# Kernel tuning notes

Hardware: AMD Instinct MI355X
Metric: run time of the kernel (lower is better)

The kernel has to match this reference:

```python
import jax, jax.numpy as jnp
import numpy as np

B, P, S = 32, 4096, 128
D_INT, D_VC, D_PATCH, H = 512, 512, 768, 4
D_CONCAT = D_INT + D_VC
D_HEAD = D_CONCAT // H  # 256
TEMPERATURE = 1.0


def setup_inputs() -> dict:
    key = jax.random.key(0)
    ks = jax.random.split(key, 9)
    h_int = jax.random.normal(ks[0], (B, D_INT), dtype=jnp.float32)
    h_vc = jax.random.normal(ks[1], (B, D_VC), dtype=jnp.float32)
    patch_tokens = jax.random.normal(ks[2], (B, P, D_PATCH), dtype=jnp.float32)
    boundaries = jnp.sort(jax.random.randint(ks[3], (S + 1,), 0, P, dtype=jnp.int32))
    # Per-head projection weights (nn.Linear: y = x @ W.T + b)
    qW = jax.random.normal(ks[4], (H, D_HEAD, D_CONCAT), dtype=jnp.float32) / np.sqrt(D_CONCAT)
    qb = jax.random.normal(ks[5], (H, D_HEAD), dtype=jnp.float32) * 0.01
    kW = jax.random.normal(ks[6], (H, D_HEAD, D_PATCH), dtype=jnp.float32) / np.sqrt(D_PATCH)
    kb = jax.random.normal(ks[7], (H, D_HEAD), dtype=jnp.float32) * 0.01
    return {"h_int": h_int, "h_vc": h_vc, "patch_tokens": patch_tokens,
            "boundaries": boundaries, "qW": qW, "qb": qb, "kW": kW, "kb": kb}


def reference(h_int, h_vc, patch_tokens, boundaries, qW, qb, kW, kb):
    b, p, _ = patch_tokens.shape
    s = boundaries.shape[0] - 1
    h_concat = jnp.concatenate([h_int, h_vc], axis=-1)            # [B, d_concat]
    # All heads at once (equivalent to the per-head Python loop)
    q = jnp.einsum('bc,hdc->bhd', h_concat, qW) + qb              # [B, H, d_head]
    k = jnp.einsum('bpc,hdc->bphd', patch_tokens, kW) + kb        # [B, P, H, d_head]
    patch_scores = jnp.einsum('bhd,bphd->bph', q, k)              # [B, P, H]
    # Map each patch to its stroke segment; out-of-range -> dump bucket s
    pos = jnp.arange(p)
    seg = jnp.searchsorted(boundaries, pos, side='right') - 1     # [P]
    seg = jnp.where((seg < 0) | (seg >= s), s, seg)
    st = patch_scores.transpose(1, 0, 2)                          # [P, B, H]
    ssum = jax.ops.segment_sum(st, seg, num_segments=s + 1)[:s]   # [S, B, H]
    cnt = jax.ops.segment_sum(jnp.ones((p,), st.dtype), seg, num_segments=s + 1)[:s]  # [S]
    stroke_scores = ssum / jnp.maximum(cnt, 1.0)[:, None, None]   # mean over patches; 0 if empty
    avg_scores = stroke_scores.mean(axis=-1).transpose(1, 0)      # [B, S] (mean over heads)
    return jax.nn.sigmoid(avg_scores / TEMPERATURE)
```

## Files before the change

### kernel.cpp

```cpp
#include <hip/hip_runtime.h>
#include <math.h>

#define NB 32
#define NP 4096
#define NS 128
#define DI 512
#define DV 512
#define DP 768
#define NH 4
#define DC 1024
#define DH 256

typedef float f4 __attribute__((ext_vector_type(4)));

__global__ __launch_bounds__(256) void k_q2(const float* __restrict__ h_int,
                                            const float* __restrict__ h_vc,
                                            const float* __restrict__ qW,
                                            const float* __restrict__ qb,
                                            const float* __restrict__ kb,
                                            float* __restrict__ q,
                                            float* __restrict__ bavg_part,
                                            float* __restrict__ acc) {
    int b = blockIdx.x >> 4, g = blockIdx.x & 15;
    int tid = threadIdx.x;

    int zi = blockIdx.x * 256 + tid;
    if (zi < NB * (NS + 1)) acc[zi] = 0.f;

    __shared__ float hc[DC];
    for (int i = tid; i < DI; i += 256) hc[i] = h_int[b * DI + i];
    for (int i = tid; i < DV; i += 256) hc[DI + i] = h_vc[b * DV + i];
    __syncthreads();

    int j = tid >> 2, r = tid & 3;
    int o = g * 64 + j;
    const float* w = qW + (size_t)o * DC + r * 256;
    const float* hq = hc + r * 256;
    float s = 0.f;
#pragma unroll 8
    for (int c = 0; c < 256; c += 4) {
        f4 wv = *(const f4*)(w + c);
        s += wv.x * hq[c] + wv.y * hq[c + 1] + wv.z * hq[c + 2] + wv.w * hq[c + 3];
    }
    s += __shfl_xor(s, 1);
    s += __shfl_xor(s, 2);
    float qv = s + qb[o];

    __shared__ float red[64];
    if (r == 0) {
        q[(size_t)b * (NH * DH) + o] = qv;
        red[j] = qv * kb[o];
    }
    __syncthreads();
    if (tid == 0) {
        float t = 0.f;
        for (int i = 0; i < 64; ++i) t += red[i];
        bavg_part[b * 16 + g] = t;
    }
}

__global__ __launch_bounds__(256) void k_w2(const float* __restrict__ q,
                                            const float* __restrict__ kW,
                                            float* __restrict__ w_part) {
    int bid = blockIdx.x;
    int cc = bid % 3, bh = bid / 3;
    int h = bh % NH, b = bh / NH;
    int tid = threadIdx.x;

    __shared__ float qs[DH];
    __shared__ f4 part[4][64];
    if (tid < DH) qs[tid] = q[(size_t)b * (NH * DH) + h * DH + tid];
    __syncthreads();

    int rc = tid >> 6, cg = tid & 63;
    const float* kbase = kW + (size_t)(h * DH + rc * 64) * DP + cc * 256 + cg * 4;
    const float* qr = qs + rc * 64;
    f4 wacc = 0.f;
#pragma unroll 8
    for (int i = 0; i < 64; ++i) {
        f4 kv = *(const f4*)(kbase + (size_t)i * DP);
        wacc += qr[i] * kv;
    }
    part[rc][cg] = wacc;
    __syncthreads();
    if (rc == 0) {
        f4 t = (part[0][cg] + part[1][cg]) + (part[2][cg] + part[3][cg]);
        *(f4*)(w_part + (size_t)(b * NH + h) * DP + cc * 256 + cg * 4) =
            t * (1.0f / NH);
    }
}

__global__ __launch_bounds__(256, 4) void k_score(const float* __restrict__ patch,
                                                  const float* __restrict__ w_part,
                                                  const int* __restrict__ bnd,
                                                  float* __restrict__ acc) {
    constexpr int CHUNKS = 32;
    constexpr int PPB = NP / CHUNKS;
    constexpr int PPW = PPB / 4;
    constexpr int RS = DP / 4;
    int b = blockIdx.x / CHUNKS;
    int chunk = blockIdx.x % CHUNKS;
    __shared__ int bsh[NS + 1];
    int tid = threadIdx.x;
    if (tid <= NS) bsh[tid] = bnd[tid];
    __syncthreads();
    int wave = tid >> 6, lane = tid & 63;

    const f4* wp = (const f4*)(w_part + (size_t)b * NH * DP);
    f4 w0 = 0.f, w1 = 0.f, w2 = 0.f;
#pragma unroll
    for (int h = 0; h < NH; ++h) {
        w0 += wp[h * RS + lane];
        w1 += wp[h * RS + 64 + lane];
        w2 += wp[h * RS + 128 + lane];
    }
    float* accb = acc + (size_t)b * (NS + 1);

    int p0 = chunk * PPB + wave * PPW;

    int cur, nxt;
    if (p0 < bsh[0]) {
        cur = NS; nxt = bsh[0];
    } else {
        int lo = 0, hi = NS;
        while (lo < hi) {
            int mid = (lo + hi + 1) >> 1;
            if (bsh[mid] <= p0) lo = mid; else hi = mid - 1;
        }
        cur = lo;
        nxt = (cur < NS) ? bsh[cur + 1] : NP;
    }

    f4 r0 = 0.f, r1 = 0.f, r2 = 0.f;
    const f4* base = (const f4*)(patch + ((size_t)b * NP + p0) * DP);

#define LOADROW(dst0, dst1, dst2, i)                                          \
    {                                                                         \
        const f4* rp_ = base + (size_t)(i) * RS;                              \
        dst0 = __builtin_nontemporal_load(rp_ + lane);                        \
        dst1 = __builtin_nontemporal_load(rp_ + 64 + lane);                   \
        dst2 = __builtin_nontemporal_load(rp_ + 128 + lane);                  \
    }

#define PROCROW(s0, s1, s2, i)                                                \
    {                                                                         \
        int p_ = p0 + (i);                                                    \
        if (p_ >= nxt) {        \
            f4 sv = r0 * w0 + r1 * w1 + r2 * w2;                              \
            float s = sv.x + sv.y + sv.z + sv.w;                              \
            for (int off_ = 32; off_ > 0; off_ >>= 1) s += __shfl_xor(s, off_); \
            if (lane == 0) atomicAdd(&accb[cur], s);                          \
            r0 = 0.f; r1 = 0.f; r2 = 0.f;                                     \
            cur = (cur == NS) ? 0 : cur + 1;                                  \
            while (cur < NS && bsh[cur + 1] <= p_) cur++;                     \
            nxt = (cur < NS) ? bsh[cur + 1] : NP;                             \
        }                                                                     \
        r0 += s0; r1 += s1; r2 += s2;                                         \
    }

    f4 A0, A1, A2, B0, B1, B2, C0, C1, C2, D0, D1, D2;
    LOADROW(A0, A1, A2, 0)
    LOADROW(B0, B1, B2, 1)
#pragma unroll
    for (int g2 = 0; g2 < PPW - 2; g2 += 2) {
        LOADROW(C0, C1, C2, g2 + 2)
        LOADROW(D0, D1, D2, g2 + 3)
        PROCROW(A0, A1, A2, g2)
        PROCROW(B0, B1, B2, g2 + 1)
        A0 = C0; A1 = C1; A2 = C2;
        B0 = D0; B1 = D1; B2 = D2;
    }
    PROCROW(A0, A1, A2, PPW - 2)
    PROCROW(B0, B1, B2, PPW - 1)

    {
        f4 sv = r0 * w0 + r1 * w1 + r2 * w2;
        float s = sv.x + sv.y + sv.z + sv.w;
#pragma unroll
        for (int off = 32; off > 0; off >>= 1) s += __shfl_xor(s, off);
        if (lane == 0) atomicAdd(&accb[cur], s);
    }
#undef LOADROW
#undef PROCROW
}

__global__ __launch_bounds__(256) void k_out(const float* __restrict__ acc,
                                             const float* __restrict__ bavg_part,
                                             const int* __restrict__ bnd,
                                             float* __restrict__ out) {
    int i = blockIdx.x * 256 + threadIdx.x;
    if (i >= NB * NS) return;
    int b = i / NS, s = i % NS;
    int cnt = bnd[s + 1] - bnd[s];
    float v = 0.f;
    if (cnt > 0) {
        float bb = 0.f;
#pragma unroll
        for (int g = 0; g < 16; ++g) bb += bavg_part[b * 16 + g];
        v = acc[b * (NS + 1) + s] / (float)cnt + bb * (1.0f / NH);
    }
    out[i] = 1.0f / (1.0f + expf(-v));
}

extern "C" void kernel_launch(void* const* d_in, const int* in_sizes, int n_in,
                              void* d_out, int out_size, void* d_ws, size_t ws_size,
                              hipStream_t stream) {
    const float* h_int = (const float*)d_in[0];
    const float* h_vc  = (const float*)d_in[1];
    const float* patch = (const float*)d_in[2];
    const int*   bnd   = (const int*)d_in[3];
    const float* qW    = (const float*)d_in[4];
    const float* qb    = (const float*)d_in[5];
    const float* kW    = (const float*)d_in[6];
    const float* kb    = (const float*)d_in[7];
    float* out = (float*)d_out;

    float* acc       = (float*)d_ws;
    float* w_part    = acc + NB * (NS + 1);
    float* bavg_part = w_part + NB * NH * DP;
    float* q         = bavg_part + NB * 16;

    k_q2<<<NB * 16, 256, 0, stream>>>(h_int, h_vc, qW, qb, kb, q, bavg_part, acc);
    k_w2<<<NB * NH * 3, 256, 0, stream>>>(q, kW, w_part);
    k_score<<<NB * 32, 256, 0, stream>>>(patch, w_part, bnd, acc);
    k_out<<<(NB * NS + 255) / 256, 256, 0, stream>>>(acc, bavg_part, bnd, out);
}
```

Measured before the change: 92.34 us.

## Reassign score work to one patch per wave across all batches, fold heads in w kernel

The score kernel now gives each wave a single patch index and loops over all 32 batches, computing the segment once with a binary search and issuing one atomic per batch per patch. Before, each wave streamed a contiguous run of patches within one batch and accumulated per segment. The w kernel now sums the four heads itself, producing a single averaged weight vector per batch, so the score kernel no longer has to add per-head partials. The new layout means many more atomics (one per patch per batch) and strided batch-stride reads per wave. It also shrinks the w kernel grid to 96 blocks, each doing four times the work.

```diff
diff --git a/kernel.cpp b/kernel.cpp
--- a/kernel.cpp
+++ b/kernel.cpp
@@ -59,129 +59,95 @@
     }
 }
 
-__global__ __launch_bounds__(256) void k_w2(const float* __restrict__ q,
+__global__ __launch_bounds__(256) void k_w3(const float* __restrict__ q,
                                             const float* __restrict__ kW,
-                                            float* __restrict__ w_part) {
+                                            float* __restrict__ w_avg) {
     int bid = blockIdx.x;
-    int cc = bid % 3, bh = bid / 3;
-    int h = bh % NH, b = bh / NH;
+    int cc = bid % 3, b = bid / 3;
     int tid = threadIdx.x;
 
-    __shared__ float qs[DH];
+    __shared__ float qs[NH * DH];
     __shared__ f4 part[4][64];
-    if (tid < DH) qs[tid] = q[(size_t)b * (NH * DH) + h * DH + tid];
+    for (int i = tid; i < NH * DH; i += 256) qs[i] = q[(size_t)b * (NH * DH) + i];
     __syncthreads();
 
     int rc = tid >> 6, cg = tid & 63;
-    const float* kbase = kW + (size_t)(h * DH + rc * 64) * DP + cc * 256 + cg * 4;
-    const float* qr = qs + rc * 64;
     f4 wacc = 0.f;
+#pragma unroll
+    for (int h = 0; h < NH; ++h) {
+        const float* kbase = kW + (size_t)(h * DH + rc * 64) * DP + cc * 256 + cg * 4;
+        const float* qr = qs + h * DH + rc * 64;
 #pragma unroll 8
-    for (int i = 0; i < 64; ++i) {
-        f4 kv = *(const f4*)(kbase + (size_t)i * DP);
-        wacc += qr[i] * kv;
+        for (int i = 0; i < 64; ++i) {
+            f4 kv = *(const f4*)(kbase + (size_t)i * DP);
+            wacc += qr[i] * kv;
+        }
     }
     part[rc][cg] = wacc;
     __syncthreads();
     if (rc == 0) {
         f4 t = (part[0][cg] + part[1][cg]) + (part[2][cg] + part[3][cg]);
-        *(f4*)(w_part + (size_t)(b * NH + h) * DP + cc * 256 + cg * 4) =
-            t * (1.0f / NH);
+        *(f4*)(w_avg + (size_t)b * DP + cc * 256 + cg * 4) = t * (1.0f / NH);
     }
 }
 
 __global__ __launch_bounds__(256, 4) void k_score(const float* __restrict__ patch,
-                                                  const float* __restrict__ w_part,
+                                                  const float* __restrict__ w_avg,
                                                   const int* __restrict__ bnd,
                                                   float* __restrict__ acc) {
-    constexpr int CHUNKS = 32;
-    constexpr int PPB = NP / CHUNKS;
-    constexpr int PPW = PPB / 4;
     constexpr int RS = DP / 4;
-    int b = blockIdx.x / CHUNKS;
-    int chunk = blockIdx.x % CHUNKS;
+    constexpr int BSTR = NP * RS;
     __shared__ int bsh[NS + 1];
     int tid = threadIdx.x;
     if (tid <= NS) bsh[tid] = bnd[tid];
     __syncthreads();
     int wave = tid >> 6, lane = tid & 63;
+    int p = blockIdx.x * 4 + wave;
 
-    const f4* wp = (const f4*)(w_part + (size_t)b * NH * DP);
-    f4 w0 = 0.f, w1 = 0.f, w2 = 0.f;
-#pragma unroll
-    for (int h = 0; h < NH; ++h) {
-        w0 += wp[h * RS + lane];
-        w1 += wp[h * RS + 64 + lane];
-        w2 += wp[h * RS + 128 + lane];
-    }
-    float* accb = acc + (size_t)b * (NS + 1);
-
-    int p0 = chunk * PPB + wave * PPW;
-
-    int cur, nxt;
-    if (p0 < bsh[0]) {
-        cur = NS; nxt = bsh[0];
+    int seg;
+    if (p < bsh[0]) {
+        seg = NS;
     } else {
         int lo = 0, hi = NS;
         while (lo < hi) {
             int mid = (lo + hi + 1) >> 1;
-            if (bsh[mid] <= p0) lo = mid; else hi = mid - 1;
+            if (bsh[mid] <= p) lo = mid; else hi = mid - 1;
         }
-        cur = lo;
-        nxt = (cur < NS) ? bsh[cur + 1] : NP;
+        seg = lo;
     }
 
-    f4 r0 = 0.f, r1 = 0.f, r2 = 0.f;
-    const f4* base = (const f4*)(patch + ((size_t)b * NP + p0) * DP);
+    const f4* prow = (const f4*)patch + (size_t)p * RS;
+    const f4* wrow = (const f4*)w_avg;
 
-#define LOADROW(dst0, dst1, dst2, i)                                          \
-    {                                                                         \
-        const f4* rp_ = base + (size_t)(i) * RS;                              \
-        dst0 = __builtin_nontemporal_load(rp_ + lane);                        \
-        dst1 = __builtin_nontemporal_load(rp_ + 64 + lane);                   \
-        dst2 = __builtin_nontemporal_load(rp_ + 128 + lane);                  \
-    }
+    f4 v0 = __builtin_nontemporal_load(prow + lane);
+    f4 v1 = __builtin_nontemporal_load(prow + 64 + lane);
+    f4 v2 = __builtin_nontemporal_load(prow + 128 + lane);
+    f4 u0 = wrow[lane], u1 = wrow[64 + lane], u2 = wrow[128 + lane];
 
-#define PROCROW(s0, s1, s2, i)                                                \
-    {                                                                         \
-        int p_ = p0 + (i);                                                    \
-        if (p_ >= nxt) {        \
-            f4 sv = r0 * w0 + r1 * w1 + r2 * w2;                              \
-            float s = sv.x + sv.y + sv.z + sv.w;                              \
-            for (int off_ = 32; off_ > 0; off_ >>= 1) s += __shfl_xor(s, off_); \
-            if (lane == 0) atomicAdd(&accb[cur], s);                          \
-            r0 = 0.f; r1 = 0.f; r2 = 0.f;                                     \
-            cur = (cur == NS) ? 0 : cur + 1;                                  \
-            while (cur < NS && bsh[cur + 1] <= p_) cur++;                     \
-            nxt = (cur < NS) ? bsh[cur + 1] : NP;                             \
-        }                                                                     \
-        r0 += s0; r1 += s1; r2 += s2;                                         \
-    }
+    for (int t = 0; t < NB - 1; ++t) {
+        const f4* np_ = prow + (size_t)(t + 1) * BSTR;
+        const f4* nw_ = wrow + (size_t)(t + 1) * RS;
+        f4 n0 = __builtin_nontemporal_load(np_ + lane);
+        f4 n1 = __builtin_nontemporal_load(np_ + 64 + lane);
+        f4 n2 = __builtin_nontemporal_load(np_ + 128 + lane);
+        f4 m0 = nw_[lane], m1 = nw_[64 + lane], m2 = nw_[128 + lane];
 
-    f4 A0, A1, A2, B0, B1, B2, C0, C1, C2, D0, D1, D2;
-    LOADROW(A0, A1, A2, 0)
-    LOADROW(B0, B1, B2, 1)
-#pragma unroll
-    for (int g2 = 0; g2 < PPW - 2; g2 += 2) {
-        LOADROW(C0, C1, C2, g2 + 2)
-        LOADROW(D0, D1, D2, g2 + 3)
-        PROCROW(A0, A1, A2, g2)
-        PROCROW(B0, B1, B2, g2 + 1)
-        A0 = C0; A1 = C1; A2 = C2;
-        B0 = D0; B1 = D1; B2 = D2;
-    }
-    PROCROW(A0, A1, A2, PPW - 2)
-    PROCROW(B0, B1, B2, PPW - 1)
-
-    {
-        f4 sv = r0 * w0 + r1 * w1 + r2 * w2;
+        f4 sv = v0 * u0 + v1 * u1 + v2 * u2;
         float s = sv.x + sv.y + sv.z + sv.w;
 #pragma unroll
         for (int off = 32; off > 0; off >>= 1) s += __shfl_xor(s, off);
-        if (lane == 0) atomicAdd(&accb[cur], s);
+        if (lane == 0) atomicAdd(&acc[t * (NS + 1) + seg], s);
+
+        v0 = n0; v1 = n1; v2 = n2;
+        u0 = m0; u1 = m1; u2 = m2;
     }
-#undef LOADROW
-#undef PROCROW
+    {
+        f4 sv = v0 * u0 + v1 * u1 + v2 * u2;
+        float s = sv.x + sv.y + sv.z + sv.w;
+#pragma unroll
+        for (int off = 32; off > 0; off >>= 1) s += __shfl_xor(s, off);
+        if (lane == 0) atomicAdd(&acc[(NB - 1) * (NS + 1) + seg], s);
+    }
 }
 
 __global__ __launch_bounds__(256) void k_out(const float* __restrict__ acc,
@@ -216,12 +182,12 @@
     float* out = (float*)d_out;
 
     float* acc       = (float*)d_ws;
-    float* w_part    = acc + NB * (NS + 1);
-    float* bavg_part = w_part + NB * NH * DP;
+    float* w_avg     = acc + NB * (NS + 1);
+    float* bavg_part = w_avg + NB * DP;
     float* q         = bavg_part + NB * 16;
 
     k_q2<<<NB * 16, 256, 0, stream>>>(h_int, h_vc, qW, qb, kb, q, bavg_part, acc);
-    k_w2<<<NB * NH * 3, 256, 0, stream>>>(q, kW, w_part);
-    k_score<<<NB * 32, 256, 0, stream>>>(patch, w_part, bnd, acc);
+    k_w3<<<NB * 3, 256, 0, stream>>>(q, kW, w_avg);
+    k_score<<<NP / 4, 256, 0, stream>>>(patch, w_avg, bnd, acc);
     k_out<<<(NB * NS + 255) / 256, 256, 0, stream>>>(acc, bavg_part, bnd, out);
 }
```

Measured after the change: 125.1 us. 1.36x slower.
